# Kernel tuning notes

Hardware: AMD Instinct MI355X
Metric: run time of the kernel (lower is better)

The kernel has to match this reference:

```python
import jax, jax.numpy as jnp
import numpy as np

S, H, NH, I = 4096, 2048, 16, 5504
HD = H // NH
EPS = 1e-6
ROPE_BASE = 10000.0


def setup_inputs() -> dict:
    key = jax.random.key(0)
    ks = jax.random.split(key, 10)
    sc = lambda fan_in: 1.0 / np.sqrt(fan_in)
    return {
        "x": jax.random.normal(ks[0], (S, H), jnp.float32),
        "wq": jax.random.normal(ks[1], (H, H), jnp.float32) * sc(H),
        "wk": jax.random.normal(ks[2], (H, H), jnp.float32) * sc(H),
        "wv": jax.random.normal(ks[3], (H, H), jnp.float32) * sc(H),
        "wo": jax.random.normal(ks[4], (H, H), jnp.float32) * sc(H),
        "w_gate": jax.random.normal(ks[5], (H, I), jnp.float32) * sc(H),
        "w_up": jax.random.normal(ks[6], (H, I), jnp.float32) * sc(H),
        "w_down": jax.random.normal(ks[7], (I, H), jnp.float32) * sc(I),
        "g1": jnp.ones((H,), jnp.float32),
        "g2": jnp.ones((H,), jnp.float32),
    }


def _rmsnorm(x, g):
    var = jnp.mean(x * x, axis=-1, keepdims=True)
    return x * jax.lax.rsqrt(var + EPS) * g


def _rope(x):
    # x: [S, NH, HD]; classic interleaved-pair rotation applied per position.
    pos = jnp.arange(S, dtype=jnp.float32)
    inv_freq = 1.0 / (ROPE_BASE ** (jnp.arange(0, HD, 2, dtype=jnp.float32) / HD))
    ang = pos[:, None] * inv_freq[None, :]              # [S, HD/2]
    cos = jnp.cos(ang)[:, None, :]                      # [S, 1, HD/2]
    sin = jnp.sin(ang)[:, None, :]
    xe = x[..., 0::2]
    xo = x[..., 1::2]
    out = jnp.stack([xe * cos - xo * sin, xe * sin + xo * cos], axis=-1)
    return out.reshape(x.shape)


def _block(x, wq, wk, wv, wo, w_gate, w_up, w_down, g1, g2):
    # --- attention sublayer ---
    h = _rmsnorm(x, g1)
    q = _rope((h @ wq).reshape(S, NH, HD))
    k = _rope((h @ wk).reshape(S, NH, HD))
    v = (h @ wv).reshape(S, NH, HD)
    scores = jnp.einsum("snd,tnd->nst", q, k) / np.sqrt(HD).astype(np.float32)
    causal = jnp.tril(jnp.ones((S, S), bool))
    scores = jnp.where(causal[None], scores, jnp.finfo(scores.dtype).min)
    probs = jax.nn.softmax(scores, axis=-1)
    attn = jnp.einsum("nst,tnd->snd", probs, v).reshape(S, H)
    x = x + attn @ wo
    # --- MLP sublayer (SwiGLU) ---
    h = _rmsnorm(x, g2)
    mlp = (jax.nn.silu(h @ w_gate) * (h @ w_up)) @ w_down
    return x + mlp


def reference(x, wq, wk, wv, wo, w_gate, w_up, w_down, g1, g2):
    return _block(x, wq, wk, wv, wo, w_gate, w_up, w_down, g1, g2)
```

## Files before the change

kernel.cpp:

```cpp
#include <hip/hip_runtime.h>
#include <stdint.h>

constexpr int SEQ  = 4096;
constexpr int HID  = 2048;
constexpr int NHEAD = 16;
constexpr int HDIM = 128;
constexpr int INTER = 5504;
constexpr int IPAD  = 5632;

using u16 = unsigned short;
typedef __bf16 bf16x8 __attribute__((ext_vector_type(8)));
typedef float  f32x4  __attribute__((ext_vector_type(4)));
typedef u16    u16x4  __attribute__((ext_vector_type(4)));
typedef u16    u16x8  __attribute__((ext_vector_type(8)));

__device__ __forceinline__ u16 f2bf(float f) {
  union { float f; unsigned u; } v; v.f = f;
  return (u16)((v.u + 0x7fffu + ((v.u >> 16) & 1u)) >> 16);
}
__device__ __forceinline__ float bf2f(u16 u) {
  union { unsigned u; float f; } v; v.u = ((unsigned)u) << 16;
  return v.f;
}

__device__ __forceinline__ unsigned cvtpk(float lo, float hi) {
  unsigned r;
  asm("v_cvt_pk_bf16_f32 %0, %1, %2" : "=v"(r) : "v"(lo), "v"(hi));
  return r;
}

__device__ __forceinline__ void gl16(const u16* g, u16* l) {
  u16* gg = const_cast<u16*>(g);
  __builtin_amdgcn_global_load_lds(
      (__attribute__((address_space(1))) u16*)gg,
      (__attribute__((address_space(3))) u16*)l, 16, 0, 0);
}

__device__ __forceinline__ f32x4 mfma16(bf16x8 a, bf16x8 b, f32x4 c) {
  return __builtin_amdgcn_mfma_f32_16x16x32_bf16(a, b, c, 0, 0, 0);
}

__global__ __launch_bounds__(256)
void fill_k(float* __restrict__ o, float v, int n) {
  int i = blockIdx.x * 256 + threadIdx.x;
  if (i < n) o[i] = v;
}

__global__ __launch_bounds__(256)
void rmsnorm_k(const float* __restrict__ x, const float* __restrict__ g,
               u16* __restrict__ o) {
  const int row = blockIdx.x, t = threadIdx.x;
  const float4* xr = (const float4*)(x + (size_t)row * HID);
  float4 a = xr[t * 2], b = xr[t * 2 + 1];
  float ss = a.x*a.x + a.y*a.y + a.z*a.z + a.w*a.w
           + b.x*b.x + b.y*b.y + b.z*b.z + b.w*b.w;
  #pragma unroll
  for (int m = 32; m; m >>= 1) ss += __shfl_xor(ss, m);
  __shared__ float red[4];
  if ((t & 63) == 0) red[t >> 6] = ss;
  __syncthreads();
  const float inv = rsqrtf((red[0]+red[1]+red[2]+red[3]) * (1.0f/HID) + 1e-6f);
  float vals[8] = {a.x,a.y,a.z,a.w,b.x,b.y,b.z,b.w};
  const int base = t * 8;
  u16x8 w;
  #pragma unroll
  for (int i = 0; i < 8; ++i) w[i] = f2bf(vals[i] * inv * g[base + i]);
  *(u16x8*)(o + (size_t)row * HID + base) = w;
}

__global__ __launch_bounds__(256)
void wtrans_k(const float* __restrict__ in, u16* __restrict__ out,
              int ldin, int ldout, int Rin, int Cin) {
  __shared__ float tile[32][33];
  const int cb = blockIdx.x * 32, rb = blockIdx.y * 32;
  const int t = threadIdx.x;
  const int c = t >> 3, r4 = (t & 7) * 4;
  if (rb >= Rin || cb >= Cin) {
    u16x4 z = {0, 0, 0, 0};
    *(u16x4*)(out + (size_t)(cb + c) * ldout + rb + r4) = z;
    return;
  }
  const int r = t >> 3, c4 = (t & 7) * 4;
  float4 v = *(const float4*)(in + (size_t)(rb + r) * ldin + cb + c4);
  tile[r][c4] = v.x; tile[r][c4+1] = v.y; tile[r][c4+2] = v.z; tile[r][c4+3] = v.w;
  __syncthreads();
  u16x4 o;
  #pragma unroll
  for (int i = 0; i < 4; ++i) o[i] = f2bf(tile[r4 + i][c]);
  *(u16x4*)(out + (size_t)(cb + c) * ldout + rb + r4) = o;
}

__global__ __launch_bounds__(256)
void vtrans_k(const u16* __restrict__ v, u16* __restrict__ vt) {
  __shared__ u16 tile[32][36];
  const int s0 = blockIdx.x * 32, d0 = blockIdx.y * 32, n = blockIdx.z;
  const int t = threadIdx.x;
  const int r = t >> 3, c4 = (t & 7) * 4;
  u16x4 in = *(const u16x4*)(v + (size_t)(s0 + r) * HID + n * HDIM + d0 + c4);
  tile[r][c4] = in[0]; tile[r][c4+1] = in[1]; tile[r][c4+2] = in[2]; tile[r][c4+3] = in[3];
  __syncthreads();
  const int d = t >> 3, s4 = (t & 7) * 4;
  u16x4 o;
  #pragma unroll
  for (int i = 0; i < 4; ++i) o[i] = tile[s4 + i][d];
  *(u16x4*)(vt + ((size_t)n * HDIM + d0 + d) * SEQ + s0 + s4) = o;
}

__global__ __launch_bounds__(256)
void rope_k(u16* __restrict__ x) {
  const int idx = blockIdx.x * 256 + threadIdx.x;
  const int i  = idx & 63;
  const int sn = idx >> 6;
  const int s  = sn >> 4;
  const size_t base = (size_t)sn * HDIM + 2 * i;
  const float xe = bf2f(x[base]), xo = bf2f(x[base + 1]);
  const float inv_freq = exp2f(-(float)i * (13.287712379549449f / 64.0f));
  const float ang = (float)s * inv_freq;
  float sv, cv;
  sincosf(ang, &sv, &cv);
  x[base]     = f2bf(xe * cv - xo * sv);
  x[base + 1] = f2bf(xe * sv + xo * cv);
}

template<int EPI>
__global__ __launch_bounds__(256)
void gemm128(const u16* __restrict__ A, const u16* __restrict__ B,
             void* C, const void* extra, int M, int N, int K, int gx) {
  __shared__ __align__(16) u16 As[128 * 64];
  __shared__ __align__(16) u16 Bs[128 * 64];
  const int bid = blockIdx.x;
  const int cid = bid & 7;
  const int idx = bid >> 3;
  const int grp = idx >> 4, win = idx & 15;
  const int bx = grp * 4 + (win & 3);
  const int by = cid * 4 + (win >> 2);
  (void)gx;
  const int m0 = by * 128, n0 = bx * 128;
  const int tid = threadIdx.x;
  const int w = tid >> 6, lane = tid & 63;
  const int l15 = lane & 15, g = lane >> 4;
  const int wr = w >> 1, wc = w & 1;
  const int NT = K >> 6;

  f32x4 acc[4][4] = {};

  const int srow = tid >> 3;
  const int sgr  = ((tid & 7) ^ (srow & 7)) * 8;
  const u16* gA = A + (size_t)(m0 + srow) * K + sgr;
  const u16* gB = B + (size_t)(n0 + srow) * K + sgr;
  const size_t i32K = (size_t)32 * K;
  const int sl = w * 512;

  const int axor = l15 & 7;
  const int arow0 = (wr * 64 + l15) * 64;
  const int brow0 = (wc * 64 + l15) * 64;

  for (int T = 0; T < NT; ++T) {
    const size_t k0 = (size_t)T * 64;
    gl16(gA + k0,            As + 0 * 2048 + sl);
    gl16(gA + k0 +     i32K, As + 1 * 2048 + sl);
    gl16(gA + k0 + 2 * i32K, As + 2 * 2048 + sl);
    gl16(gA + k0 + 3 * i32K, As + 3 * 2048 + sl);
    gl16(gB + k0,            Bs + 0 * 2048 + sl);
    gl16(gB + k0 +     i32K, Bs + 1 * 2048 + sl);
    gl16(gB + k0 + 2 * i32K, Bs + 2 * 2048 + sl);
    gl16(gB + k0 + 3 * i32K, Bs + 3 * 2048 + sl);
    asm volatile("s_waitcnt vmcnt(0)" ::: "memory");
    __syncthreads();
    #pragma unroll
    for (int ks = 0; ks < 2; ++ks) {
      const int aoff = ((ks * 4 + g) ^ axor) * 8;
      bf16x8 af[4], bfr[4];
      #pragma unroll
      for (int i = 0; i < 4; ++i)
        af[i] = *(const bf16x8*)&As[arow0 + i * 16 * 64 + aoff];
      #pragma unroll
      for (int j = 0; j < 4; ++j)
        bfr[j] = *(const bf16x8*)&Bs[brow0 + j * 16 * 64 + aoff];
      #pragma unroll
      for (int i = 0; i < 4; ++i)
        #pragma unroll
        for (int j = 0; j < 4; ++j)
          acc[i][j] = mfma16(af[i], bfr[j], acc[i][j]);
    }
    asm volatile("s_waitcnt lgkmcnt(0)" ::: "memory");
    __syncthreads();
  }

  #pragma unroll
  for (int i = 0; i < 4; ++i) {
    #pragma unroll
    for (int r = 0; r < 4; ++r) {
      const int row = m0 + wr * 64 + i * 16 + g * 4 + r;
      #pragma unroll
      for (int j = 0; j < 4; ++j) {
        const int col = n0 + wc * 64 + j * 16 + l15;
        const float v = acc[i][j][r];
        if constexpr (EPI == 0) {
          ((u16*)C)[(size_t)(col >> 11) * ((size_t)SEQ * HID)
                    + (size_t)row * HID + (col & 2047)] = f2bf(v);
        } else if constexpr (EPI == 1) {
          const size_t idx2 = (size_t)row * N + col;
          ((float*)C)[idx2] = v + ((const float*)extra)[idx2];
        } else if constexpr (EPI == 2) {
          const size_t idx2 = (size_t)row * N + col;
          const float upv = bf2f(((const u16*)extra)[idx2]);
          ((u16*)C)[idx2] = f2bf(v / (1.0f + __expf(-v)) * upv);
        } else {
          ((u16*)C)[(size_t)row * N + col] = f2bf(v);
        }
      }
    }
  }
}

__global__ __launch_bounds__(256)
void attn_k(const u16* __restrict__ q, const u16* __restrict__ k,
            const u16* __restrict__ vt, u16* __restrict__ o) {
  __shared__ __align__(16) u16 Ks[64 * 128];
  __shared__ __align__(16) u16 Vs[128 * 64];
  __shared__ __align__(16) u16 Ps[4 * 16 * 64];
  const int b = blockIdx.x;
  const int n    = ((b & 7) << 1) | ((b >> 3) & 1);
  const int qIdx = 63 - (b >> 4);
  const int q0   = qIdx * 64;
  const int tid = threadIdx.x;
  const int wave = tid >> 6, lane = tid & 63;
  const int l15 = lane & 15, g = lane >> 4;

  bf16x8 aq[4];
  {
    const u16* qp = q + (size_t)(q0 + wave*16 + l15) * HID + n * HDIM + g * 8;
    #pragma unroll
    for (int d = 0; d < 4; ++d) aq[d] = *(const bf16x8*)(qp + d * 32);
  }
  float mrow[4];
  #pragma unroll
  for (int r = 0; r < 4; ++r) mrow[r] = -__builtin_inff();
  f32x4 oacc[8] = {};
  f32x4 lacc = {0.0f, 0.0f, 0.0f, 0.0f};
  const bf16x8 vone = {(__bf16)1.0f, (__bf16)1.0f, (__bf16)1.0f, (__bf16)1.0f,
                       (__bf16)1.0f, (__bf16)1.0f, (__bf16)1.0f, (__bf16)1.0f};

  const int kRow = tid >> 4;
  const int kCs  = (tid & 15) ^ (kRow & 7);
  const u16* kg = k + (size_t)kRow * HID + n * HDIM + kCs * 8;
  const int vRow = tid >> 3;
  const int vCs  = (tid & 7) ^ (vRow & 7);
  const u16* vg = vt + ((size_t)n * HDIM + vRow) * SEQ + vCs * 8;

  u16* PW = Ps + wave * 1024;
  const int rsw = (l15 & 7) << 3;
  const float C = 0.12751744f;

  const int nt = qIdx + 1;
  for (int it = 0; it < nt; ++it) {
    const int t0 = it * 64;
    #pragma unroll
    for (int s = 0; s < 4; ++s)
      gl16(kg + (size_t)(t0 + s*16) * HID, Ks + s*2048 + wave*512);
    #pragma unroll
    for (int s = 0; s < 4; ++s)
      gl16(vg + (size_t)(s*32) * SEQ + t0, Vs + s*2048 + wave*512);
    asm volatile("s_waitcnt vmcnt(0)" ::: "memory");
    __syncthreads();

    f32x4 sc[4] = {};
    #pragma unroll
    for (int tb = 0; tb < 4; ++tb) {
      #pragma unroll
      for (int dd = 0; dd < 4; ++dd) {
        bf16x8 bk = *(const bf16x8*)(Ks + (tb*16 + l15)*128 + ((dd*32 + g*8) ^ rsw));
        sc[tb] = mfma16(aq[dd], bk, sc[tb]);
      }
    }

    const bool diag = (it == qIdx);
    #pragma unroll
    for (int r = 0; r < 4; ++r) {
      float v0 = sc[0][r], v1 = sc[1][r], v2 = sc[2][r], v3 = sc[3][r];
      if (diag) {
        const int srow = q0 + wave*16 + g*4 + r;
        const int tt = t0 + l15;
        if (tt      > srow) v0 = -__builtin_inff();
        if (tt + 16 > srow) v1 = -__builtin_inff();
        if (tt + 32 > srow) v2 = -__builtin_inff();
        if (tt + 48 > srow) v3 = -__builtin_inff();
      }
      float mx = fmaxf(fmaxf(v0, v1), fmaxf(v2, v3));
      mx = fmaxf(mx, __shfl_xor(mx, 1));
      mx = fmaxf(mx, __shfl_xor(mx, 2));
      mx = fmaxf(mx, __shfl_xor(mx, 4));
      mx = fmaxf(mx, __shfl_xor(mx, 8));
      if (mx > mrow[r] + 60.0f) {
        const float f = exp2f((mrow[r] - mx) * C);
        mrow[r] = mx;
        lacc[r] *= f;
        #pragma unroll
        for (int db = 0; db < 8; ++db) oacc[db][r] *= f;
      }
      const float m = mrow[r];
      const float p0 = exp2f((v0 - m) * C);
      const float p1 = exp2f((v1 - m) * C);
      const float p2 = exp2f((v2 - m) * C);
      const float p3 = exp2f((v3 - m) * C);
      const unsigned pk01 = cvtpk(p0, p1);
      const unsigned pk23 = cvtpk(p2, p3);
      const int prow = g*4 + r;
      const int psw = (prow & 7) << 3;
      PW[prow*64 + ( l15        ^ psw)] = (u16)pk01;
      PW[prow*64 + ((16 + l15)  ^ psw)] = (u16)(pk01 >> 16);
      PW[prow*64 + ((32 + l15)  ^ psw)] = (u16)pk23;
      PW[prow*64 + ((48 + l15)  ^ psw)] = (u16)(pk23 >> 16);
    }

    bf16x8 ap0 = *(const bf16x8*)(PW + l15*64 + ((g*8)      ^ rsw));
    bf16x8 ap1 = *(const bf16x8*)(PW + l15*64 + ((32 + g*8) ^ rsw));
    lacc = mfma16(ap0, vone, lacc);
    lacc = mfma16(ap1, vone, lacc);
    #pragma unroll
    for (int db = 0; db < 8; ++db) {
      bf16x8 bv0 = *(const bf16x8*)(Vs + (db*16 + l15)*64 + ((g*8)      ^ rsw));
      bf16x8 bv1 = *(const bf16x8*)(Vs + (db*16 + l15)*64 + ((32 + g*8) ^ rsw));
      oacc[db] = mfma16(ap0, bv0, oacc[db]);
      oacc[db] = mfma16(ap1, bv1, oacc[db]);
    }
    asm volatile("s_waitcnt lgkmcnt(0)" ::: "memory");
    __syncthreads();
  }

  #pragma unroll
  for (int db = 0; db < 8; ++db) {
    #pragma unroll
    for (int r = 0; r < 4; ++r) {
      const int srow = q0 + wave*16 + g*4 + r;
      o[(size_t)srow * HID + n * HDIM + db*16 + l15] = f2bf(oacc[db][r] / lacc[r]);
    }
  }
}

extern "C" void kernel_launch(void* const* d_in, const int* in_sizes, int n_in,
                              void* d_out, int out_size, void* d_ws, size_t ws_size,
                              hipStream_t stream) {
  (void)in_sizes; (void)n_in; (void)out_size;
  const float* x  = (const float*)d_in[0];
  const float* wq = (const float*)d_in[1];
  const float* wk = (const float*)d_in[2];
  const float* wv = (const float*)d_in[3];
  const float* wo = (const float*)d_in[4];
  const float* wg = (const float*)d_in[5];
  const float* wu = (const float*)d_in[6];
  const float* wd = (const float*)d_in[7];
  const float* g1 = (const float*)d_in[8];
  const float* g2 = (const float*)d_in[9];
  float* out = (float*)d_out;

  constexpr size_t HB  = (size_t)SEQ * HID * 2;
  constexpr size_t WT  = (size_t)HID * HID * 2;
  constexpr size_t WUP = (size_t)IPAD * HID * 2;
  constexpr size_t UPH = (size_t)SEQ * IPAD * 2;
  constexpr size_t NEED1 = 4 * HB + 3 * WT;
  constexpr size_t NEED2 = HB + WUP + UPH;
  constexpr size_t NEED = NEED1 > NEED2 ? NEED1 : NEED2;

  if (ws_size < NEED) {
    const int n = SEQ * HID;
    fill_k<<<dim3((n + 255) / 256), 256, 0, stream>>>(out, (float)(ws_size >> 20), n);
    return;
  }

  char* base = (char*)d_ws;
  u16* h1     = (u16*)(base);
  u16* wqkvT  = (u16*)(base + HB);
  u16* qb     = (u16*)(base + HB + 3 * WT);
  u16* kb     = (u16*)(base + 2 * HB + 3 * WT);
  u16* vb     = (u16*)(base + 3 * HB + 3 * WT);
  u16* vtb    = h1;
  u16* ob     = vb;
  u16* woT    = wqkvT;
  u16* h2    = (u16*)(base);
  u16* slotA = (u16*)(base + HB);
  u16* uph   = (u16*)(base + HB + WUP);

  wtrans_k<<<dim3(64, 64), 256, 0, stream>>>(wq, wqkvT,            HID, HID, HID, HID);
  wtrans_k<<<dim3(64, 64), 256, 0, stream>>>(wk, wqkvT + HID*HID,  HID, HID, HID, HID);
  wtrans_k<<<dim3(64, 64), 256, 0, stream>>>(wv, wqkvT + 2*HID*HID,HID, HID, HID, HID);

  rmsnorm_k<<<dim3(SEQ), 256, 0, stream>>>(x, g1, h1);

  gemm128<0><<<dim3(1536), 256, 0, stream>>>(h1, wqkvT, qb, nullptr, SEQ, 3*HID, HID, 48);

  rope_k<<<dim3(SEQ * NHEAD * 64 / 256), 256, 0, stream>>>(qb);
  rope_k<<<dim3(SEQ * NHEAD * 64 / 256), 256, 0, stream>>>(kb);

  vtrans_k<<<dim3(SEQ/32, HDIM/32, NHEAD), 256, 0, stream>>>(vb, vtb);

  wtrans_k<<<dim3(64, 64), 256, 0, stream>>>(wo, woT, HID, HID, HID, HID);

  attn_k<<<dim3(SEQ/64 * NHEAD), 256, 0, stream>>>(qb, kb, vtb, ob);

  gemm128<1><<<dim3(512), 256, 0, stream>>>(ob, woT, out, x, SEQ, HID, HID, 16);

  rmsnorm_k<<<dim3(SEQ), 256, 0, stream>>>(out, g2, h2);

  wtrans_k<<<dim3(IPAD/32, 64), 256, 0, stream>>>(wu, slotA, INTER, HID, HID, INTER);
  gemm128<3><<<dim3(1408), 256, 0, stream>>>(h2, slotA, uph, nullptr, SEQ, IPAD, HID, 44);

  wtrans_k<<<dim3(IPAD/32, 64), 256, 0, stream>>>(wg, slotA, INTER, HID, HID, INTER);
  gemm128<2><<<dim3(1408), 256, 0, stream>>>(h2, slotA, uph, uph, SEQ, IPAD, HID, 44);

  wtrans_k<<<dim3(64, IPAD/32), 256, 0, stream>>>(wd, slotA, HID, IPAD, INTER, HID);
  gemm128<1><<<dim3(512), 256, 0, stream>>>(uph, slotA, out, out, SEQ, HID, IPAD, 16);
}
```

Baseline: 834.0 us.

## Add 128x64-tile GEMM for N=2048 projections and raise MFMA priority in attention

Adds a GEMM variant with 128x64 output tiles and uses it for the output projection and down projection. With N=2048 these launches go from 512 to 1024 workgroups, which is meant to fill the 256 CUs more evenly. It also wraps the attention kernel's MFMA sections in s_setprio so matrix work gets scheduling priority over other waves. The smaller tiles cost more A-operand reloads per output element and give less reuse per workgroup.

```diff
diff --git a/kernel.cpp b/kernel.cpp
--- a/kernel.cpp
+++ b/kernel.cpp
@@ -214,6 +214,89 @@
   }
 }
 
+template<int EPI>
+__global__ __launch_bounds__(256)
+void gemm128n64(const u16* __restrict__ A, const u16* __restrict__ B,
+                void* C, const void* extra, int M, int N, int K, int gx) {
+  __shared__ __align__(16) u16 As[128 * 64];
+  __shared__ __align__(16) u16 Bs[64 * 64];
+  const int bid = blockIdx.x;
+  const int cid = bid & 7;
+  const int idx = bid >> 3;
+  const int grp = idx >> 4, win = idx & 15;
+  const int bx = grp * 4 + (win & 3);
+  const int by = cid * 4 + (win >> 2);
+  (void)gx;
+  const int m0 = by * 128, n0 = bx * 64;
+  const int tid = threadIdx.x;
+  const int w = tid >> 6, lane = tid & 63;
+  const int l15 = lane & 15, g = lane >> 4;
+  const int wr = w >> 1, wc = w & 1;
+  const int NT = K >> 6;
+
+  f32x4 acc[4][2] = {};
+
+  const int srow = tid >> 3;
+  const int sgr  = ((tid & 7) ^ (srow & 7)) * 8;
+  const u16* gA = A + (size_t)(m0 + srow) * K + sgr;
+  const u16* gB = B + (size_t)(n0 + srow) * K + sgr;
+  const size_t i32K = (size_t)32 * K;
+  const int sl = w * 512;
+
+  const int axor = l15 & 7;
+  const int arow0 = (wr * 64 + l15) * 64;
+  const int brow0 = (wc * 32 + l15) * 64;
+
+  for (int T = 0; T < NT; ++T) {
+    const size_t k0 = (size_t)T * 64;
+    gl16(gA + k0,            As + 0 * 2048 + sl);
+    gl16(gA + k0 +     i32K, As + 1 * 2048 + sl);
+    gl16(gA + k0 + 2 * i32K, As + 2 * 2048 + sl);
+    gl16(gA + k0 + 3 * i32K, As + 3 * 2048 + sl);
+    gl16(gB + k0,            Bs + 0 * 2048 + sl);
+    gl16(gB + k0 +     i32K, Bs + 1 * 2048 + sl);
+    asm volatile("s_waitcnt vmcnt(0)" ::: "memory");
+    __syncthreads();
+    #pragma unroll
+    for (int ks = 0; ks < 2; ++ks) {
+      const int aoff = ((ks * 4 + g) ^ axor) * 8;
+      bf16x8 af[4], bfr[2];
+      #pragma unroll
+      for (int i = 0; i < 4; ++i)
+        af[i] = *(const bf16x8*)&As[arow0 + i * 16 * 64 + aoff];
+      #pragma unroll
+      for (int j = 0; j < 2; ++j)
+        bfr[j] = *(const bf16x8*)&Bs[brow0 + j * 16 * 64 + aoff];
+      #pragma unroll
+      for (int i = 0; i < 4; ++i)
+        #pragma unroll
+        for (int j = 0; j < 2; ++j)
+          acc[i][j] = mfma16(af[i], bfr[j], acc[i][j]);
+    }
+    asm volatile("s_waitcnt lgkmcnt(0)" ::: "memory");
+    __syncthreads();
+  }
+
+  #pragma unroll
+  for (int i = 0; i < 4; ++i) {
+    #pragma unroll
+    for (int r = 0; r < 4; ++r) {
+      const int row = m0 + wr * 64 + i * 16 + g * 4 + r;
+      #pragma unroll
+      for (int j = 0; j < 2; ++j) {
+        const int col = n0 + wc * 32 + j * 16 + l15;
+        const float v = acc[i][j][r];
+        if constexpr (EPI == 1) {
+          const size_t idx2 = (size_t)row * N + col;
+          ((float*)C)[idx2] = v + ((const float*)extra)[idx2];
+        } else {
+          ((u16*)C)[(size_t)row * N + col] = f2bf(v);
+        }
+      }
+    }
+  }
+}
+
 __global__ __launch_bounds__(256)
 void attn_k(const u16* __restrict__ q, const u16* __restrict__ k,
             const u16* __restrict__ vt, u16* __restrict__ o) {
@@ -266,6 +349,7 @@
     __syncthreads();
 
     f32x4 sc[4] = {};
+    __builtin_amdgcn_s_setprio(1);
     #pragma unroll
     for (int tb = 0; tb < 4; ++tb) {
       #pragma unroll
@@ -274,6 +358,7 @@
         sc[tb] = mfma16(aq[dd], bk, sc[tb]);
       }
     }
+    __builtin_amdgcn_s_setprio(0);
 
     const bool diag = (it == qIdx);
     #pragma unroll
@@ -316,6 +401,7 @@
 
     bf16x8 ap0 = *(const bf16x8*)(PW + l15*64 + ((g*8)      ^ rsw));
     bf16x8 ap1 = *(const bf16x8*)(PW + l15*64 + ((32 + g*8) ^ rsw));
+    __builtin_amdgcn_s_setprio(1);
     lacc = mfma16(ap0, vone, lacc);
     lacc = mfma16(ap1, vone, lacc);
     #pragma unroll
@@ -325,6 +411,7 @@
       oacc[db] = mfma16(ap0, bv0, oacc[db]);
       oacc[db] = mfma16(ap1, bv1, oacc[db]);
     }
+    __builtin_amdgcn_s_setprio(0);
     asm volatile("s_waitcnt lgkmcnt(0)" ::: "memory");
     __syncthreads();
   }
@@ -399,7 +486,7 @@
 
   attn_k<<<dim3(SEQ/64 * NHEAD), 256, 0, stream>>>(qb, kb, vtb, ob);
 
-  gemm128<1><<<dim3(512), 256, 0, stream>>>(ob, woT, out, x, SEQ, HID, HID, 16);
+  gemm128n64<1><<<dim3(1024), 256, 0, stream>>>(ob, woT, out, x, SEQ, HID, HID, 32);
 
   rmsnorm_k<<<dim3(SEQ), 256, 0, stream>>>(out, g2, h2);
 
@@ -410,5 +497,5 @@
   gemm128<2><<<dim3(1408), 256, 0, stream>>>(h2, slotA, uph, uph, SEQ, IPAD, HID, 44);
 
   wtrans_k<<<dim3(64, IPAD/32), 256, 0, stream>>>(wd, slotA, HID, IPAD, INTER, HID);
-  gemm128<1><<<dim3(512), 256, 0, stream>>>(uph, slotA, out, out, SEQ, HID, IPAD, 16);
-}
+  gemm128n64<1><<<dim3(1024), 256, 0, stream>>>(uph, slotA, out, out, SEQ, HID, IPAD, 32);
+}
```

After: 829.1 us. No clear change (-0.6%).
